# Performance work log

Measured on AMD Instinct MI355X. Metric: run time of the kernel, lower is better.

## Reference

```python
import jax, jax.numpy as jnp
import numpy as np

N, E, C, S = 30000, 480000, 256, 4
T_EVO = 0.1        # evolution_time
MAX_EIG = 0.5      # max_eigenval in create_ultra_stable_hamiltonian
MAX_NORM = 0.01    # max_norm in ultra_stable_matrix_exp
MAX_TERMS = 4
LN_EPS = 1e-5


def _build_subgraphs(edge_index, n, s):
    """Emulates the per-node k_hop=1 BFS (capped at max_subgraph_size=s) and the
    subgraph laplacian Hamiltonian build (edge_weight=0.1, self-loops added).
    Pure structural preprocessing: integer/constant w.r.t. all float params."""
    src = np.asarray(edge_index[0], dtype=np.int64)
    dst = np.asarray(edge_index[1], dtype=np.int64)
    loops = np.arange(n, dtype=np.int64)
    src = np.concatenate([src, loops]); dst = np.concatenate([dst, loops])
    order = np.argsort(src, kind='stable')
    src_s, dst_s = src[order], dst[order]
    starts = np.searchsorted(src_s, np.arange(n))
    ends = np.searchsorted(src_s, np.arange(n) + 1)
    edge_set = set((src * n + dst).tolist())
    sub_nodes = np.zeros((n, s), dtype=np.int64)
    sub_mask = np.zeros((n, s), dtype=np.float32)
    H = np.zeros((n, s, s), dtype=np.float32)
    for i in range(n):
        nbrs = [i]
        for d in dst_s[starts[i]:ends[i]]:
            d = int(d)
            if d != i and d not in nbrs:
                nbrs.append(d)
                if len(nbrs) == s:
                    break
        m = len(nbrs)
        sub_nodes[i, :m] = nbrs
        sub_nodes[i, m:] = i          # pad with center (masked out below)
        sub_mask[i, :m] = 1.0
        A = np.zeros((s, s), dtype=np.float32)
        for a in range(m):
            ka = nbrs[a] * n
            for b in range(m):
                if (ka + nbrs[b]) in edge_set:
                    A[a, b] = 1.0
        deg = np.maximum(A.sum(axis=1), 1e-6)   # degree(row), clamped like torch
        H[i] = np.diag(deg) - 0.1 * A           # laplacian with edge_weight=0.1
    return sub_nodes, sub_mask, H


def _mat_fro(M):
    return jnp.sqrt(jnp.sum(jnp.abs(M) ** 2, axis=(-2, -1)))


def _unitary_from_H(sub_H):
    """ultra_stable_matrix_exp, batched over N tiny [S,S] Hamiltonians.
    The torch .item() norm/eigenvalue rescales detach gradients, so treating this
    whole block as parameter-independent (it is: H is structural) is faithful."""
    Hc = sub_H.astype(jnp.complex64)
    ev = jnp.linalg.eigvals(Hc)                              # [N,S] (CPU op)
    mx = jnp.max(ev.real, axis=-1)
    Hc = Hc * jnp.where(mx > MAX_EIG, MAX_EIG / mx, 1.0)[:, None, None]
    hn = _mat_fro(Hc)
    Hc = Hc * jnp.where(hn > MAX_NORM, MAX_NORM / hn, 1.0)[:, None, None]
    A = (-1j) * Hc * (T_EVO * 0.1)                           # scaled_H
    I = jnp.eye(S, dtype=jnp.complex64)
    U = jnp.broadcast_to(I, Hc.shape)
    term = U
    for k in range(1, MAX_TERMS + 1):
        term = jnp.matmul(term, A) / k
        tn = _mat_fro(term)
        term = term * jnp.where(tn > 0.1, 0.1 / tn, 1.0)[:, None, None]
        U = U + term
    err = _mat_fro(jnp.matmul(U, jnp.conj(jnp.swapaxes(U, -1, -2))) - I)
    U = jnp.where((err > 0.1)[:, None, None], I + A * 0.01, U)
    return U


def _cplx_linear(xr, xi, wr, wi, br, bi):
    xr = jnp.clip(xr, -10.0, 10.0); xi = jnp.clip(xi, -10.0, 10.0)
    re = xr @ wr.T - xi @ wi.T + br
    im = xr @ wi.T + xi @ wr.T + bi
    return re + 1j * im


def _cln(z, w, b, eps=LN_EPS):
    # UltraStableComplexLayerNorm, training-mode batch stats over dim 0
    mag = jnp.clip(jnp.sqrt(z.real ** 2 + z.imag ** 2 + eps), eps, 1000.0)
    mean = mag.mean(0)
    var = mag.var(0)
    nm = (mag - mean) / (jnp.sqrt(var + eps) + eps)
    sm = jnp.clip(nm * jnp.abs(w) + b, eps, 10.0)
    ph = jnp.arctan2(jnp.clip(z.imag, -1e6, 1e6), jnp.clip(z.real, -1e6, 1e6) + 1e-10)
    return sm * jnp.cos(ph) + 1j * (sm * jnp.sin(ph))


def _crelu(z, leak=0.01, mx=5.0):
    r = jnp.clip(z.real, -mx, mx); i = jnp.clip(z.imag, -mx, mx)
    return jnp.where(r > 0, r, leak * r) + 1j * jnp.where(i > 0, i, leak * i)


def setup_inputs() -> dict:
    key = jax.random.key(0)
    k1, k2, k3, k4 = jax.random.split(key, 4)
    x = jax.random.normal(k1, (N, C), dtype=jnp.float32)
    edge_index = jax.random.randint(k2, (2, E), 0, N, dtype=jnp.int64)
    sub_nodes, sub_mask, sub_H = _build_subgraphs(np.asarray(edge_index), N, S)
    std = np.sqrt(0.5 / C).astype(np.float32)
    w_real = jax.random.normal(k3, (C, C), dtype=jnp.float32) * std
    w_imag = jax.random.normal(k4, (C, C), dtype=jnp.float32) * std
    return {
        'x': x,
        'edge_index': edge_index,
        'sub_nodes': jnp.asarray(sub_nodes),
        'sub_mask': jnp.asarray(sub_mask),
        'sub_H': jnp.asarray(sub_H),
        'w_real': w_real,
        'w_imag': w_imag,
        'b_real': jnp.zeros((C,), jnp.float32),
        'b_imag': jnp.zeros((C,), jnp.float32),
        'ln_weight': jnp.full((C,), 0.1, jnp.float32),
        'ln_bias': jnp.zeros((C,), jnp.float32),
        'evolution_scale': jnp.asarray(0.1, jnp.float32),
    }


def reference(x, edge_index, sub_nodes, sub_mask, sub_H,
              w_real, w_imag, b_real, b_imag, ln_weight, ln_bias,
              evolution_scale):
    # complex linear (input is real -> imag part zero, matching torch.complex(x, 0*x))
    h = _cplx_linear(x, jnp.zeros_like(x), w_real, w_imag, b_real, b_imag)  # [N,C] c64
    U = _unitary_from_H(sub_H)                                              # [N,S,S]
    sub_x = h[sub_nodes] * sub_mask[..., None]                              # [N,S,C]
    # center node is slot 0 of each subgraph -> take row 0 of U @ sub_x
    evolved = jnp.einsum('ns,nsc->nc', U[:, 0, :], sub_x)
    out = evolved * evolution_scale + x.astype(jnp.complex64)  # residual (in==out)
    out = _cln(out, ln_weight, ln_bias)
    out = _crelu(out)
    # dropout is eval-mode identity
    return jnp.concatenate([out.real, out.imag], axis=-1)      # [N, 2C] float32
```

## Files before the change

kernel.cpp:

```cpp
#include <hip/hip_runtime.h>
#include <stdint.h>

#define N_NODES 30000
#define NC 256

typedef _Float16 f16x8 __attribute__((ext_vector_type(8)));
typedef _Float16 f16x4 __attribute__((ext_vector_type(4)));
typedef _Float16 f16x2 __attribute__((ext_vector_type(2)));
typedef float f32x4 __attribute__((ext_vector_type(4)));

#define NBX 7500
#define NBW 128
#define NBP 118
__global__ __launch_bounds__(256) void k_pre(
    const float* __restrict__ x, _Float16* __restrict__ xb,
    const float* __restrict__ wr, const float* __restrict__ wi,
    _Float16* __restrict__ Wb,
    const float* __restrict__ subH, const float* __restrict__ sub_mask,
    const float* __restrict__ escp, float* __restrict__ c4,
    float* __restrict__ ssum, float* __restrict__ ssumsq)
{
    int bid = blockIdx.x, tid = threadIdx.x;
    if (bid < NBX) {
        int i = (bid * 256 + tid) * 4;
        float4 v = *reinterpret_cast<const float4*>(x + i);
        f16x4 o;
        o[0] = (_Float16)fminf(fmaxf(v.x, -10.f), 10.f);
        o[1] = (_Float16)fminf(fmaxf(v.y, -10.f), 10.f);
        o[2] = (_Float16)fminf(fmaxf(v.z, -10.f), 10.f);
        o[3] = (_Float16)fminf(fmaxf(v.w, -10.f), 10.f);
        *reinterpret_cast<f16x4*>(xb + i) = o;
    } else if (bid < NBX + NBW) {
        int i = ((bid - NBX) * 256 + tid) * 4;
        const float* src = (i < NC * NC) ? (wr + i) : (wi + (i - NC * NC));
        float4 v = *reinterpret_cast<const float4*>(src);
        f16x4 o;
        o[0] = (_Float16)v.x; o[1] = (_Float16)v.y;
        o[2] = (_Float16)v.z; o[3] = (_Float16)v.w;
        *reinterpret_cast<f16x4*>(Wb + i) = o;
    } else if (bid < NBX + NBW + NBP) {
        int node = (bid - NBX - NBW) * 256 + tid;
        if (node < N_NODES) {
            float esc = *escp;
            const float4* Hp = reinterpret_cast<const float4*>(subH + node * 16);
            float4 r0 = Hp[0], r1 = Hp[1], r2 = Hp[2], r3 = Hp[3];
            float fr = r0.x * r0.x + r0.y * r0.y + r0.z * r0.z + r0.w * r0.w
                     + r1.x * r1.x + r1.y * r1.y + r1.z * r1.z + r1.w * r1.w
                     + r2.x * r2.x + r2.y * r2.y + r2.z * r2.z + r2.w * r2.w
                     + r3.x * r3.x + r3.y * r3.y + r3.z * r3.z + r3.w * r3.w;
            float coef = 1e-4f * rsqrtf(fr) * esc;
            float4 m = *reinterpret_cast<const float4*>(sub_mask + node * 4);
            float4 o;
            o.x = coef * r0.x * m.x;
            o.y = coef * r0.y * m.y;
            o.z = coef * r0.z * m.z;
            o.w = coef * r0.w * m.w;
            *reinterpret_cast<float4*>(c4 + node * 4) = o;
        }
    } else {
        ssum[tid] = 0.f;
        ssumsq[tid] = 0.f;
    }
}

__global__ __launch_bounds__(256, 2) void k_gemm(
    const _Float16* __restrict__ A, const _Float16* __restrict__ B,
    const float* __restrict__ br, const float* __restrict__ bi,
    _Float16* __restrict__ H)
{
    int bid = blockIdx.x;
    int bm = bid >> 1, cs = bid & 1;
    int tid = threadIdx.x;
    int lane = tid & 63, wave = tid >> 6;
    int quad = lane >> 4, l16 = lane & 15;
    int wm = wave >> 1, wn = wave & 1;
    int row0 = bm * 128 + wm * 64;

    f16x8 af[4][8];
#pragma unroll
    for (int mi = 0; mi < 4; mi++) {
        int r = row0 + mi * 16 + l16;
        if (r >= N_NODES) r = N_NODES - 1;
        const _Float16* ap = A + r * NC + quad * 8;
#pragma unroll
        for (int kc = 0; kc < 8; kc++)
            af[mi][kc] = *reinterpret_cast<const f16x8*>(ap + kc * 32);
    }

    const float* bias_p = wn ? bi : br;
#pragma unroll
    for (int cn = 0; cn < 2; cn++) {
        const _Float16* bbase = B + ((wn ? 256 : 0) + cs * 128 + cn * 64 + l16) * NC
                                  + quad * 8;
        f16x8 bb[2][4];
#pragma unroll
        for (int ni = 0; ni < 4; ni++)
            bb[0][ni] = *reinterpret_cast<const f16x8*>(bbase + ni * 16 * NC);
        f32x4 acc[4][4] = {};
#pragma unroll
        for (int kc = 0; kc < 8; kc++) {
            int cur = kc & 1, nxt = cur ^ 1;
            if (kc < 7) {
#pragma unroll
                for (int ni = 0; ni < 4; ni++)
                    bb[nxt][ni] = *reinterpret_cast<const f16x8*>(
                        bbase + ni * 16 * NC + (kc + 1) * 32);
            }
#pragma unroll
            for (int mi = 0; mi < 4; mi++)
#pragma unroll
                for (int ni = 0; ni < 4; ni++)
                    acc[mi][ni] = __builtin_amdgcn_mfma_f32_16x16x32_f16(
                        af[mi][kc], bb[cur][ni], acc[mi][ni], 0, 0, 0);
        }
#pragma unroll
        for (int ni = 0; ni < 4; ni++) {
            int c = cs * 128 + cn * 64 + ni * 16 + l16;
            float bias = bias_p[c];
            int cc = 2 * c + wn;
#pragma unroll
            for (int mi = 0; mi < 4; mi++) {
                int rowb = row0 + mi * 16 + quad * 4;
#pragma unroll
                for (int r = 0; r < 4; r++) {
                    int row = rowb + r;
                    if (row < N_NODES)
                        H[row * 512 + cc] = (_Float16)(acc[mi][ni][r] + bias);
                }
            }
        }
    }
}

#define NPB 60
#define NGRP 8
__global__ __launch_bounds__(512) void k_evolve(
    const float* __restrict__ x, const int* __restrict__ sub_nodes,
    const float* __restrict__ c4, const _Float16* __restrict__ h,
    const float* __restrict__ escp,
    float* __restrict__ outz, _Float16* __restrict__ zbuf, int use_f16,
    float* __restrict__ ssum, float* __restrict__ ssumsq)
{
    __shared__ int   s_nodes[NPB][4];
    __shared__ float s_P[NPB][4];
    __shared__ float s_redA[NGRP][256];
    __shared__ float s_redB[NGRP][256];
    int tid = threadIdx.x;
    int g = tid >> 6, lane = tid & 63;
    int base = blockIdx.x * NPB;
    if (tid < NPB) {
        int node = base + tid;
        *reinterpret_cast<float4*>(&s_P[tid][0]) =
            *reinterpret_cast<const float4*>(c4 + node * 4);
        *reinterpret_cast<int4*>(&s_nodes[tid][0]) =
            *reinterpret_cast<const int4*>(sub_nodes + node * 4);
    }
    __syncthreads();
    float esc = *escp;
    float lsum[4] = {0.f, 0.f, 0.f, 0.f};
    float lsq[4]  = {0.f, 0.f, 0.f, 0.f};

    f16x8 hvA[4];
    float4 xA;
    int j = g;
#pragma unroll
    for (int s = 0; s < 4; s++)
        hvA[s] = *reinterpret_cast<const f16x8*>(h + s_nodes[j][s] * 512 + lane * 8);
    xA = *reinterpret_cast<const float4*>(x + (base + j) * NC + lane * 4);

    for (;;) {
        int jn = j + NGRP;
        bool more = jn < NPB;
        f16x8 hvB[4];
        float4 xB;
        if (more) {
#pragma unroll
            for (int s = 0; s < 4; s++)
                hvB[s] = *reinterpret_cast<const f16x8*>(
                    h + s_nodes[jn][s] * 512 + lane * 8);
            xB = *reinterpret_cast<const float4*>(x + (base + jn) * NC + lane * 4);
        }
        {
            int node = base + j;
            float P0 = s_P[j][0], P1 = s_P[j][1], P2 = s_P[j][2], P3 = s_P[j][3];
            float xr[4] = {xA.x, xA.y, xA.z, xA.w};
            f16x8 zo;
            float or4[4], oi4[4];
#pragma unroll
            for (int e = 0; e < 4; e++) {
                float hr0 = (float)hvA[0][2 * e], hi0 = (float)hvA[0][2 * e + 1];
                float hr1 = (float)hvA[1][2 * e], hi1 = (float)hvA[1][2 * e + 1];
                float hr2 = (float)hvA[2][2 * e], hi2 = (float)hvA[2][2 * e + 1];
                float hr3 = (float)hvA[3][2 * e], hi3 = (float)hvA[3][2 * e + 1];
                float er = esc * hr0;
                float ei = esc * hi0;
                er = fmaf(P0, hi0, er); ei = fmaf(-P0, hr0, ei);
                er = fmaf(P1, hi1, er); ei = fmaf(-P1, hr1, ei);
                er = fmaf(P2, hi2, er); ei = fmaf(-P2, hr2, ei);
                er = fmaf(P3, hi3, er); ei = fmaf(-P3, hr3, ei);
                float outr = er + xr[e];
                float outi = ei;
                or4[e] = outr; oi4[e] = outi;
                zo[2 * e] = (_Float16)outr; zo[2 * e + 1] = (_Float16)outi;
                float mag = sqrtf(fmaf(outr, outr, fmaf(outi, outi, 1e-5f)));
                mag = fminf(fmaxf(mag, 1e-5f), 1000.f);
                lsum[e] += mag;
                lsq[e] = fmaf(mag, mag, lsq[e]);
            }
            if (use_f16) {
                *reinterpret_cast<f16x8*>(zbuf + node * 512 + lane * 8) = zo;
            } else {
                *reinterpret_cast<float4*>(outz + node * 512 + lane * 4) =
                    make_float4(or4[0], or4[1], or4[2], or4[3]);
                *reinterpret_cast<float4*>(outz + node * 512 + 256 + lane * 4) =
                    make_float4(oi4[0], oi4[1], oi4[2], oi4[3]);
            }
        }
        if (!more) break;
#pragma unroll
        for (int s = 0; s < 4; s++) hvA[s] = hvB[s];
        xA = xB;
        j = jn;
    }
#pragma unroll
    for (int e = 0; e < 4; e++) {
        s_redA[g][lane * 4 + e] = lsum[e];
        s_redB[g][lane * 4 + e] = lsq[e];
    }
    __syncthreads();
    if (tid < 256) {
        float a = 0.f;
#pragma unroll
        for (int q = 0; q < NGRP; q++) a += s_redA[q][tid];
        atomicAdd(&ssum[tid], a);
    } else {
        int t = tid - 256;
        float b = 0.f;
#pragma unroll
        for (int q = 0; q < NGRP; q++) b += s_redB[q][t];
        atomicAdd(&ssumsq[t], b);
    }
}

__global__ __launch_bounds__(256) void k_norm(
    float* __restrict__ out, const _Float16* __restrict__ zbuf, int use_f16,
    const float* __restrict__ ssum, const float* __restrict__ ssumsq,
    const float* __restrict__ lnw, const float* __restrict__ lnb)
{
    int tid = threadIdx.x;
    int node = blockIdx.x * 4 + (tid >> 6);
    int c0 = (tid & 63) * 4;
    float re[4], im[4];
    if (use_f16) {
        f16x8 z = *reinterpret_cast<const f16x8*>(zbuf + node * 512 + c0 * 2);
#pragma unroll
        for (int e = 0; e < 4; e++) { re[e] = (float)z[2 * e]; im[e] = (float)z[2 * e + 1]; }
    } else {
        float4 r4 = *reinterpret_cast<const float4*>(out + node * 512 + c0);
        float4 i4 = *reinterpret_cast<const float4*>(out + node * 512 + 256 + c0);
        re[0] = r4.x; re[1] = r4.y; re[2] = r4.z; re[3] = r4.w;
        im[0] = i4.x; im[1] = i4.y; im[2] = i4.z; im[3] = i4.w;
    }
    float4 s4 = *reinterpret_cast<const float4*>(ssum + c0);
    float4 q4 = *reinterpret_cast<const float4*>(ssumsq + c0);
    float4 w4 = *reinterpret_cast<const float4*>(lnw + c0);
    float4 lb4 = *reinterpret_cast<const float4*>(lnb + c0);
    float S[4] = {s4.x, s4.y, s4.z, s4.w};
    float Q[4] = {q4.x, q4.y, q4.z, q4.w};
    float W[4] = {w4.x, w4.y, w4.z, w4.w};
    float L[4] = {lb4.x, lb4.y, lb4.z, lb4.w};
    const float invN = 1.0f / (float)N_NODES;
    float orr[4], oii[4];
#pragma unroll
    for (int e = 0; e < 4; e++) {
        float mean = S[e] * invN;
        float var = fmaxf(Q[e] * invN - mean * mean, 0.f);
        float denom = sqrtf(var + 1e-5f) + 1e-5f;
        float A = fabsf(W[e]) / denom;
        float Bc = L[e] - mean * A;
        float r = re[e], i = im[e];
        float mag = sqrtf(fmaf(r, r, fmaf(i, i, 1e-5f)));
        mag = fminf(fmaxf(mag, 1e-5f), 1000.f);
        float sm = fmaf(mag, A, Bc);
        sm = fminf(fmaxf(sm, 1e-5f), 10.0f);
        float px = fminf(fmaxf(r, -1e6f), 1e6f) + 1e-10f;
        float py = fminf(fmaxf(i, -1e6f), 1e6f);
        float r2 = fmaf(px, px, py * py);
        float inv = rsqrtf(r2);
        float zr = sm * px * inv, zi = sm * py * inv;
        zr = fminf(fmaxf(zr, -5.f), 5.f);
        zi = fminf(fmaxf(zi, -5.f), 5.f);
        orr[e] = zr > 0.f ? zr : 0.01f * zr;
        oii[e] = zi > 0.f ? zi : 0.01f * zi;
    }
    *reinterpret_cast<float4*>(out + node * 512 + c0) =
        make_float4(orr[0], orr[1], orr[2], orr[3]);
    *reinterpret_cast<float4*>(out + node * 512 + 256 + c0) =
        make_float4(oii[0], oii[1], oii[2], oii[3]);
}

extern "C" void kernel_launch(void* const* d_in, const int* in_sizes, int n_in,
                              void* d_out, int out_size, void* d_ws, size_t ws_size,
                              hipStream_t stream) {
    const float* x        = (const float*)d_in[0];
    const int*   sub_nodes = (const int*)d_in[2];
    const float* sub_mask  = (const float*)d_in[3];
    const float* subH      = (const float*)d_in[4];
    const float* wr  = (const float*)d_in[5];
    const float* wi  = (const float*)d_in[6];
    const float* br  = (const float*)d_in[7];
    const float* bi  = (const float*)d_in[8];
    const float* lnw = (const float*)d_in[9];
    const float* lnb = (const float*)d_in[10];
    const float* esc = (const float*)d_in[11];
    float* out = (float*)d_out;

    char* ws = (char*)d_ws;
    const size_t XB_OFF   = 0;
    const size_t WB_OFF   = 15360000;
    const size_t H_OFF    = 15622144;
    const size_t STAT_OFF = 46342144;
    const size_t C4_OFF   = 46346240;
    const size_t ZB_OFF   = 46826240;
    const size_t WS_NEED_F16 = ZB_OFF + 30720000;
    _Float16* xb = (_Float16*)(ws + XB_OFF);
    _Float16* Wb = (_Float16*)(ws + WB_OFF);
    _Float16* h  = (_Float16*)(ws + H_OFF);
    float* ssum   = (float*)(ws + STAT_OFF);
    float* ssumsq = (float*)(ws + STAT_OFF + 1024);
    float* c4     = (float*)(ws + C4_OFF);
    _Float16* zbuf = (_Float16*)(ws + ZB_OFF);
    int use_f16 = (ws_size >= WS_NEED_F16) ? 1 : 0;

    hipLaunchKernelGGL(k_pre, dim3(NBX + NBW + NBP + 1), dim3(256), 0, stream,
                       x, xb, wr, wi, Wb, subH, sub_mask, esc, c4, ssum, ssumsq);
    hipLaunchKernelGGL(k_gemm, dim3(235 * 2), dim3(256), 0, stream, xb, Wb, br, bi, h);
    hipLaunchKernelGGL(k_evolve, dim3(500), dim3(512), 0, stream,
                       x, sub_nodes, c4, h, esc, out, zbuf, use_f16,
                       ssum, ssumsq);
    hipLaunchKernelGGL(k_norm, dim3(7500), dim3(256), 0, stream,
                       out, zbuf, use_f16, ssum, ssumsq, lnw, lnb);
}
```

Measured before the change: 193.7 us.

## Stage GEMM B tile in swizzled LDS via async global-to-LDS loads

The GEMM kernel now copies a 128x256 slice of the weight matrix (64 real and 64 imaginary output columns) into XOR-swizzled shared memory using global_load_lds. Each wave then reads its B fragments from LDS instead of from global memory. The grid grows to four column slices of 64, and the A fragments are loaded per k-chunk instead of all being held in registers. Real and imaginary results are written together as packed f16x2 stores. The goal is to cut redundant global B reads and register pressure and to coalesce the output stores, at the cost of 64KB of LDS per block, which limits occupancy, and of reading A twice as often across blocks.

After: 182.3 us (median of 2 runs). 5.9% less time.

```diff
diff --git a/kernel.cpp b/kernel.cpp
--- a/kernel.cpp
+++ b/kernel.cpp
@@ -8,6 +8,10 @@
 typedef _Float16 f16x4 __attribute__((ext_vector_type(4)));
 typedef _Float16 f16x2 __attribute__((ext_vector_type(2)));
 typedef float f32x4 __attribute__((ext_vector_type(4)));
+
+#define GLOAD_LDS16(g, l) __builtin_amdgcn_global_load_lds(                      \
+    (const __attribute__((address_space(1))) void*)(g),                          \
+    (__attribute__((address_space(3))) void*)(l), 16, 0, 0)
 
 #define NBX 7500
 #define NBW 128
@@ -68,64 +72,77 @@
     const float* __restrict__ br, const float* __restrict__ bi,
     _Float16* __restrict__ H)
 {
+    __shared__ _Float16 Bs[128 * 256];
     int bid = blockIdx.x;
-    int bm = bid >> 1, cs = bid & 1;
+    int bm = bid % 235;
+    int cs = bid / 235;
     int tid = threadIdx.x;
-    int lane = tid & 63, wave = tid >> 6;
-    int quad = lane >> 4, l16 = lane & 15;
-    int wm = wave >> 1, wn = wave & 1;
+    int wv = tid >> 6, ln = tid & 63;
+
+#pragma unroll
+    for (int i = 0; i < 16; i++) {
+        int brow = i * 8 + wv * 2 + (ln >> 5);
+        int chunk = ln & 31;
+        int Brow = (brow < 64) ? (cs * 64 + brow) : (256 + cs * 64 + brow - 64);
+        int chl = chunk ^ (brow & 7);
+        const _Float16* src = B + Brow * 256 + chl * 8;
+        GLOAD_LDS16(src, &Bs[i * 2048 + wv * 512]);
+    }
+
+    int quad = ln >> 4, l16 = ln & 15;
+    int wm = wv >> 1, wq = wv & 1;
     int row0 = bm * 128 + wm * 64;
 
-    f16x8 af[4][8];
+    const _Float16* ap[4];
 #pragma unroll
     for (int mi = 0; mi < 4; mi++) {
         int r = row0 + mi * 16 + l16;
         if (r >= N_NODES) r = N_NODES - 1;
-        const _Float16* ap = A + r * NC + quad * 8;
-#pragma unroll
-        for (int kc = 0; kc < 8; kc++)
-            af[mi][kc] = *reinterpret_cast<const f16x8*>(ap + kc * 32);
-    }
-
-    const float* bias_p = wn ? bi : br;
-#pragma unroll
-    for (int cn = 0; cn < 2; cn++) {
-        const _Float16* bbase = B + ((wn ? 256 : 0) + cs * 128 + cn * 64 + l16) * NC
-                                  + quad * 8;
-        f16x8 bb[2][4];
-#pragma unroll
-        for (int ni = 0; ni < 4; ni++)
-            bb[0][ni] = *reinterpret_cast<const f16x8*>(bbase + ni * 16 * NC);
-        f32x4 acc[4][4] = {};
-#pragma unroll
-        for (int kc = 0; kc < 8; kc++) {
-            int cur = kc & 1, nxt = cur ^ 1;
-            if (kc < 7) {
-#pragma unroll
-                for (int ni = 0; ni < 4; ni++)
-                    bb[nxt][ni] = *reinterpret_cast<const f16x8*>(
-                        bbase + ni * 16 * NC + (kc + 1) * 32);
-            }
-#pragma unroll
-            for (int mi = 0; mi < 4; mi++)
-#pragma unroll
-                for (int ni = 0; ni < 4; ni++)
-                    acc[mi][ni] = __builtin_amdgcn_mfma_f32_16x16x32_f16(
-                        af[mi][kc], bb[cur][ni], acc[mi][ni], 0, 0, 0);
-        }
+        ap[mi] = A + r * NC + quad * 8;
+    }
+    int brow_f[4];
+#pragma unroll
+    for (int ni = 0; ni < 4; ni++)
+        brow_f[ni] = (ni < 2 ? 0 : 64) + wq * 32 + (ni & 1) * 16 + l16;
+
+    __syncthreads();
+
+    f32x4 acc[4][4] = {};
+#pragma unroll
+    for (int kc = 0; kc < 8; kc++) {
+        f16x8 af[4];
+#pragma unroll
+        for (int mi = 0; mi < 4; mi++)
+            af[mi] = *reinterpret_cast<const f16x8*>(ap[mi] + kc * 32);
+        f16x8 bf[4];
 #pragma unroll
         for (int ni = 0; ni < 4; ni++) {
-            int c = cs * 128 + cn * 64 + ni * 16 + l16;
-            float bias = bias_p[c];
-            int cc = 2 * c + wn;
-#pragma unroll
-            for (int mi = 0; mi < 4; mi++) {
-                int rowb = row0 + mi * 16 + quad * 4;
-#pragma unroll
-                for (int r = 0; r < 4; r++) {
-                    int row = rowb + r;
-                    if (row < N_NODES)
-                        H[row * 512 + cc] = (_Float16)(acc[mi][ni][r] + bias);
+            int ch = (quad + kc * 4) ^ (l16 & 7);
+            bf[ni] = *reinterpret_cast<const f16x8*>(&Bs[brow_f[ni] * 256 + ch * 8]);
+        }
+#pragma unroll
+        for (int mi = 0; mi < 4; mi++)
+#pragma unroll
+            for (int ni = 0; ni < 4; ni++)
+                acc[mi][ni] = __builtin_amdgcn_mfma_f32_16x16x32_f16(
+                    af[mi], bf[ni], acc[mi][ni], 0, 0, 0);
+    }
+
+#pragma unroll
+    for (int ni = 0; ni < 2; ni++) {
+        int c = cs * 64 + wq * 32 + ni * 16 + l16;
+        float brc = br[c], bic = bi[c];
+#pragma unroll
+        for (int mi = 0; mi < 4; mi++) {
+            int rowb = row0 + mi * 16 + quad * 4;
+#pragma unroll
+            for (int r = 0; r < 4; r++) {
+                int row = rowb + r;
+                if (row < N_NODES) {
+                    f16x2 p;
+                    p[0] = (_Float16)(acc[mi][ni][r] + brc);
+                    p[1] = (_Float16)(acc[mi][ni + 2][r] + bic);
+                    *reinterpret_cast<f16x2*>(H + row * 512 + 2 * c) = p;
                 }
             }
         }
@@ -334,7 +351,7 @@
 
     hipLaunchKernelGGL(k_pre, dim3(NBX + NBW + NBP + 1), dim3(256), 0, stream,
                        x, xb, wr, wi, Wb, subH, sub_mask, esc, c4, ssum, ssumsq);
-    hipLaunchKernelGGL(k_gemm, dim3(235 * 2), dim3(256), 0, stream, xb, Wb, br, bi, h);
+    hipLaunchKernelGGL(k_gemm, dim3(235 * 4), dim3(256), 0, stream, xb, Wb, br, bi, h);
     hipLaunchKernelGGL(k_evolve, dim3(500), dim3(512), 0, stream,
                        x, sub_nodes, c4, h, esc, out, zbuf, use_f16,
                        ssum, ssumsq);
```
